# Kernel tuning notes

Hardware: AMD Instinct MI355X
Metric: run time of the kernel (lower is better)

## Reference

```python
import jax, jax.numpy as jnp
import numpy as np


def setup_inputs() -> dict:
    key = jax.random.key(0)
    k1, k2, k3 = jax.random.split(key, 3)
    B, D, C = 512, 256, 1000
    embedding = jax.random.normal(k1, (B, D), dtype=jnp.float32)
    labels = jax.random.randint(k2, (B,), 0, C, dtype=jnp.int64)
    W = jax.random.normal(k3, (C, D), dtype=jnp.float32) * 0.02
    return {"embedding": embedding, "labels": labels, "W": W}


def reference(embedding, labels, W):
    # MRL-E loss: (1/D) * sum_{k=1..D} CE(z[:, :k] @ W[:, :k].T, y)
    # Computed incrementally: logits_k = logits_{k-1} + z[:, k] outer W[:, k],
    # which is mathematically identical to recomputing the prefix matmul.
    B, D = embedding.shape
    C = W.shape[0]
    rows = jnp.arange(B)
    labels = labels.astype(jnp.int32)

    def step(logits, cols):
        z_col, w_col = cols  # [B], [C]
        logits = logits + z_col[:, None] * w_col[None, :]  # rank-1 update, [B, C]
        # stable cross-entropy: mean(logsumexp(logits) - logits[i, y_i])
        lse = jax.nn.logsumexp(logits, axis=-1)  # [B]
        lab_logit = logits[rows, labels]  # [B]
        loss_k = jnp.mean(lse - lab_logit)
        return logits, loss_k

    init = jnp.zeros((B, C), dtype=embedding.dtype)
    _, losses = jax.lax.scan(step, init, (embedding.T, W.T))  # losses: [D]
    return jnp.sum(losses) / D
```

## Files before the change

kernel.cpp:

```cpp
#include <hip/hip_runtime.h>
#include <hip/hip_bf16.h>
#include <math.h>


#define MRLE_B 512
#define MRLE_D 256
#define MRLE_C 1000
#define MRLE_CP 1024
#define MRLE_KROWS 264
#define MRLE_NT 512
#define ROWD (MRLE_CP / 2)
#define RSTR 17
#define LOG2E 1.4426950408889634f
#define LN2   0.6931471805599453f

#if __has_builtin(__builtin_amdgcn_exp2f)
#define EXP2(x) __builtin_amdgcn_exp2f(x)
#else
#define EXP2(x) __builtin_exp2f(x)
#endif

__global__ __launch_bounds__(256) void mrle_transpose(
    const float* __restrict__ W, unsigned short* __restrict__ Wtb)
{
    __shared__ float tile[64][65];
    const int c0 = blockIdx.x * 64;
    const int k0 = blockIdx.y * 64;
    const int t  = threadIdx.x;
    const int r  = t >> 2;
    const int q  = t & 3;

#pragma unroll
    for (int j = 0; j < 4; ++j) {
        const int c    = c0 + r;
        const int kcol = q * 4 + j * 16;
        float4 v = make_float4(0.f, 0.f, 0.f, 0.f);
        if (c < MRLE_C) v = *(const float4*)&W[(size_t)c * MRLE_D + k0 + kcol];
        tile[r][kcol + 0] = v.x;
        tile[r][kcol + 1] = v.y;
        tile[r][kcol + 2] = v.z;
        tile[r][kcol + 3] = v.w;
    }
    __syncthreads();

#pragma unroll
    for (int j = 0; j < 4; ++j) {
        const int cc = q * 4 + j * 16;
        unsigned short hh[4];
#pragma unroll
        for (int e = 0; e < 4; ++e) {
            const float f = tile[cc + e][r] * LOG2E;
            unsigned int u = __float_as_uint(f);
            u = (u + 0x7FFFu + ((u >> 16) & 1u)) >> 16;
            hh[e] = (unsigned short)u;
        }
        *(ushort4*)&Wtb[(size_t)(k0 + r) * MRLE_CP + c0 + cc] =
            make_ushort4(hh[0], hh[1], hh[2], hh[3]);
    }
}

__global__ __launch_bounds__(MRLE_NT) void mrle_main(
    const float* __restrict__ z,
    const int* __restrict__ labels,
    const float* __restrict__ W,
    const unsigned short* __restrict__ Wtb,
    float* __restrict__ out)
{
    __shared__ float zsh[MRLE_D];
    __shared__ float red[8 * 64 * RSTR];
    __shared__ float Sw[8 * MRLE_D];
    __shared__ float wred[8];

    const int i  = blockIdx.x;
    const int t  = threadIdx.x;
    const int wv = t >> 6;
    const int l  = t & 63;

    if (t < MRLE_D) zsh[t] = z[i * MRLE_D + t];
    __syncthreads();

    const int cbase = 2 * t;
    float l0 = (cbase     < MRLE_C) ? 0.f : -INFINITY;
    float l1 = (cbase + 1 < MRLE_C) ? 0.f : -INFINITY;

    const unsigned int* Wp = (const unsigned int*)Wtb + t;

    unsigned int wbuf[8];
#pragma unroll
    for (int q = 0; q < 8; ++q) wbuf[q] = Wp[(size_t)q * ROWD];

    float* redw = red + wv * (64 * RSTR);
    float* wr = redw + l * RSTR;
    const float* rd = redw + (l & 48) * RSTR + (l & 15);

#pragma unroll 1
    for (int cb = 0; cb < 16; ++cb) {
        float zq[16];
        *(float4*)&zq[0]  = *(const float4*)&zsh[cb * 16 + 0];
        *(float4*)&zq[4]  = *(const float4*)&zsh[cb * 16 + 4];
        *(float4*)&zq[8]  = *(const float4*)&zsh[cb * 16 + 8];
        *(float4*)&zq[12] = *(const float4*)&zsh[cb * 16 + 12];

#pragma unroll
        for (int kk4 = 0; kk4 < 4; ++kk4) {
            const unsigned int* qp =
                Wp + (size_t)(cb * 16 + kk4 * 4 + 10) * ROWD;
#pragma unroll
            for (int j = 0; j < 4; ++j) {
                const int kk = kk4 * 4 + j;
                const unsigned int w = wbuf[kk & 7];
                const float w0 = __uint_as_float(w << 16);
                const float w1 = __uint_as_float(w & 0xFFFF0000u);
                l0 = fmaf(zq[kk], w0, l0);
                l1 = fmaf(zq[kk], w1, l1);
                wr[kk] = EXP2(l0) + EXP2(l1);
                wbuf[kk & 7] = qp[(j - 2) * (int)ROWD];
            }
        }

        float s = 0.f;
#pragma unroll
        for (int u = 0; u < 16; ++u)
            s += rd[u * RSTR];
        s += __shfl_xor(s, 16);
        s += __shfl_xor(s, 32);
        if (l < 16) Sw[wv * MRLE_D + cb * 16 + l] = s;
    }

    __syncthreads();

    float v = 0.f;
    if (t < MRLE_D) {
        float S = 0.f;
#pragma unroll
        for (int wq = 0; wq < 8; ++wq) S += Sw[wq * MRLE_D + t];
        const float lse = LN2 * __log2f(S);

        const int y = labels[i];
        const float lab = zsh[t] * W[(size_t)y * MRLE_D + t] *
                          (float)(MRLE_D - t);
        v = lse - lab;
    }

#pragma unroll
    for (int d = 1; d < 64; d <<= 1) v += __shfl_xor(v, d);
    if (l == 0) wred[wv] = v;
    __syncthreads();
    if (t == 0) {
        float tot = 0.f;
#pragma unroll
        for (int wq = 0; wq < 8; ++wq) tot += wred[wq];
        atomicAdd(out, tot * (1.0f / ((float)MRLE_B * (float)MRLE_D)));
    }
}

extern "C" void kernel_launch(void* const* d_in, const int* in_sizes, int n_in,
                              void* d_out, int out_size, void* d_ws, size_t ws_size,
                              hipStream_t stream) {
    const float* z      = (const float*)d_in[0];
    const int*   labels = (const int*)d_in[1];
    const float* W      = (const float*)d_in[2];
    float*       out    = (float*)d_out;

    unsigned short* Wtb = (unsigned short*)d_ws;

    hipMemsetAsync(out, 0, sizeof(float), stream);
    mrle_transpose<<<dim3(16, 4), 256, 0, stream>>>(W, Wtb);
    mrle_main<<<MRLE_B, MRLE_NT, 0, stream>>>(z, labels, W, Wtb, out);
}
```

Baseline: 38.22 us.

## Replace LDS transpose reduction with DPP row scans and fold output zeroing

Per-lane exp sums are reduced across each 16-lane row with DPP shift-adds instead of a padded LDS scratch and shuffles. Row totals are written as 32 partials per k and summed at the end. The z row is read directly from global memory, and the output memset is moved into the transpose kernel to save a launch. Dropping the low-bit mask on w1 adds a tiny rounding perturbation.

```diff
diff --git a/kernel.cpp b/kernel.cpp
--- a/kernel.cpp
+++ b/kernel.cpp
@@ -10,7 +10,6 @@
 #define MRLE_KROWS 264
 #define MRLE_NT 512
 #define ROWD (MRLE_CP / 2)
-#define RSTR 17
 #define LOG2E 1.4426950408889634f
 #define LN2   0.6931471805599453f
 
@@ -20,8 +19,13 @@
 #define EXP2(x) __builtin_exp2f(x)
 #endif
 
+#define DPP_ADD_SHR(s, n)                                                     \
+    s += __uint_as_float((unsigned)__builtin_amdgcn_update_dpp(               \
+        0, (int)__float_as_uint(s), 0x110 + (n), 0xf, 0xf, false))
+
 __global__ __launch_bounds__(256) void mrle_transpose(
-    const float* __restrict__ W, unsigned short* __restrict__ Wtb)
+    const float* __restrict__ W, unsigned short* __restrict__ Wtb,
+    float* __restrict__ out)
 {
     __shared__ float tile[64][65];
     const int c0 = blockIdx.x * 64;
@@ -29,6 +33,8 @@
     const int t  = threadIdx.x;
     const int r  = t >> 2;
     const int q  = t & 3;
+
+    if (c0 == 0 && k0 == 0 && t == 0) out[0] = 0.f;
 
 #pragma unroll
     for (int j = 0; j < 4; ++j) {
@@ -66,9 +72,7 @@
     const unsigned short* __restrict__ Wtb,
     float* __restrict__ out)
 {
-    __shared__ float zsh[MRLE_D];
-    __shared__ float red[8 * 64 * RSTR];
-    __shared__ float Sw[8 * MRLE_D];
+    __shared__ float Sw[32 * MRLE_D];
     __shared__ float wred[8];
 
     const int i  = blockIdx.x;
@@ -76,8 +80,7 @@
     const int wv = t >> 6;
     const int l  = t & 63;
 
-    if (t < MRLE_D) zsh[t] = z[i * MRLE_D + t];
-    __syncthreads();
+    const float* zrow = z + (size_t)i * MRLE_D;
 
     const int cbase = 2 * t;
     float l0 = (cbase     < MRLE_C) ? 0.f : -INFINITY;
@@ -89,18 +92,15 @@
 #pragma unroll
     for (int q = 0; q < 8; ++q) wbuf[q] = Wp[(size_t)q * ROWD];
 
-    float* redw = red + wv * (64 * RSTR);
-    float* wr = redw + l * RSTR;
-    const float* rd = redw + (l & 48) * RSTR + (l & 15);
-
 #pragma unroll 1
     for (int cb = 0; cb < 16; ++cb) {
         float zq[16];
-        *(float4*)&zq[0]  = *(const float4*)&zsh[cb * 16 + 0];
-        *(float4*)&zq[4]  = *(const float4*)&zsh[cb * 16 + 4];
-        *(float4*)&zq[8]  = *(const float4*)&zsh[cb * 16 + 8];
-        *(float4*)&zq[12] = *(const float4*)&zsh[cb * 16 + 12];
+        *(float4*)&zq[0]  = *(const float4*)&zrow[cb * 16 + 0];
+        *(float4*)&zq[4]  = *(const float4*)&zrow[cb * 16 + 4];
+        *(float4*)&zq[8]  = *(const float4*)&zrow[cb * 16 + 8];
+        *(float4*)&zq[12] = *(const float4*)&zrow[cb * 16 + 12];
 
+        float ps[16];
 #pragma unroll
         for (int kk4 = 0; kk4 < 4; ++kk4) {
             const unsigned int* qp =
@@ -110,21 +110,31 @@
                 const int kk = kk4 * 4 + j;
                 const unsigned int w = wbuf[kk & 7];
                 const float w0 = __uint_as_float(w << 16);
-                const float w1 = __uint_as_float(w & 0xFFFF0000u);
+                const float w1 = __uint_as_float(w);
                 l0 = fmaf(zq[kk], w0, l0);
                 l1 = fmaf(zq[kk], w1, l1);
-                wr[kk] = EXP2(l0) + EXP2(l1);
+                ps[kk] = EXP2(l0) + EXP2(l1);
                 wbuf[kk & 7] = qp[(j - 2) * (int)ROWD];
             }
         }
 
-        float s = 0.f;
 #pragma unroll
-        for (int u = 0; u < 16; ++u)
-            s += rd[u * RSTR];
-        s += __shfl_xor(s, 16);
-        s += __shfl_xor(s, 32);
-        if (l < 16) Sw[wv * MRLE_D + cb * 16 + l] = s;
+        for (int kk = 0; kk < 16; ++kk) {
+            float s = ps[kk];
+            DPP_ADD_SHR(s, 1);
+            DPP_ADD_SHR(s, 2);
+            DPP_ADD_SHR(s, 4);
+            DPP_ADD_SHR(s, 8);
+            ps[kk] = s;
+        }
+
+        if ((l & 15) == 15) {
+            float4* dst = (float4*)&Sw[(((wv << 2) | (l >> 4)) * 16 + cb) * 16];
+            dst[0] = make_float4(ps[0],  ps[1],  ps[2],  ps[3]);
+            dst[1] = make_float4(ps[4],  ps[5],  ps[6],  ps[7]);
+            dst[2] = make_float4(ps[8],  ps[9],  ps[10], ps[11]);
+            dst[3] = make_float4(ps[12], ps[13], ps[14], ps[15]);
+        }
     }
 
     __syncthreads();
@@ -133,11 +143,11 @@
     if (t < MRLE_D) {
         float S = 0.f;
 #pragma unroll
-        for (int wq = 0; wq < 8; ++wq) S += Sw[wq * MRLE_D + t];
+        for (int p = 0; p < 32; ++p) S += Sw[p * MRLE_D + t];
         const float lse = LN2 * __log2f(S);
 
         const int y = labels[i];
-        const float lab = zsh[t] * W[(size_t)y * MRLE_D + t] *
+        const float lab = zrow[t] * W[(size_t)y * MRLE_D + t] *
                           (float)(MRLE_D - t);
         v = lse - lab;
     }
@@ -164,7 +174,6 @@
 
     unsigned short* Wtb = (unsigned short*)d_ws;
 
-    hipMemsetAsync(out, 0, sizeof(float), stream);
-    mrle_transpose<<<dim3(16, 4), 256, 0, stream>>>(W, Wtb);
+    mrle_transpose<<<dim3(16, 4), 256, 0, stream>>>(W, Wtb, out);
     mrle_main<<<MRLE_B, MRLE_NT, 0, stream>>>(z, labels, W, Wtb, out);
 }
```

New measurement: 47.90 us. 1.25x slower.
